# Optimization experiments

Measured on AMD Instinct MI355X. Metric: run time of the kernel, lower is better.

The kernel has to match this reference:

```python
import jax, jax.numpy as jnp
import numpy as np

IN_F, OUT_F = 4096, 4096
RANK, N_EXP, TOP_K = 8, 64, 16
R_DIM = 16
ALPHA = 32
SCALING = ALPHA / TOP_K  # 2.0
B_SZ, SEQ = 4, 4096
BOTTLENECK = N_EXP * RANK  # 512


def setup_inputs() -> dict:
    key = jax.random.key(0)
    kx, ka, kb, kq, kk = jax.random.split(key, 5)
    x = jax.random.normal(kx, (B_SZ, SEQ, IN_F), dtype=jnp.float32)
    # A: kaiming-uniform-like; B: torch inits to zeros but we use small random
    # values so the output / gradients are non-degenerate for kernel testing.
    A_w = jax.random.normal(ka, (BOTTLENECK, IN_F), dtype=jnp.float32) * (1.0 / np.sqrt(IN_F))
    B_w = jax.random.normal(kb, (OUT_F, BOTTLENECK), dtype=jnp.float32) * 0.02
    Wq_w = jax.random.normal(kq, (R_DIM, IN_F), dtype=jnp.float32) * (1.0 / np.sqrt(IN_F))
    keys = jax.random.normal(kk, (N_EXP, R_DIM), dtype=jnp.float32) * 0.01
    return {"x": x, "A_w": A_w, "B_w": B_w, "Wq_w": Wq_w, "keys": keys}


def reference(x, A_w, B_w, Wq_w, keys):
    # dropout p=0 -> identity
    # shared A projection: [b,s,d] @ [d, E*r] -> [b,s,E,r]
    z = jnp.einsum('bsd,ed->bse', x, A_w).reshape(B_SZ, SEQ, N_EXP, RANK)
    # lowrank router: scores = (x @ Wq.T) @ keys.T -> [b,s,E]
    q = jnp.einsum('bsd,rd->bsr', x, Wq_w)
    scores = jnp.einsum('bsr,er->bse', q, keys)
    top_scores, top_idx = jax.lax.top_k(scores, TOP_K)          # [b,s,k]
    top_w = jax.nn.softmax(top_scores, axis=-1)                  # [b,s,k]
    # dense gate [b,s,E] via scatter of softmaxed top-k weights
    gate = jnp.sum(jax.nn.one_hot(top_idx, N_EXP, dtype=top_w.dtype)
                   * top_w[..., None], axis=-2)                  # [b,s,E]
    z_gated = (z * gate[..., None]).reshape(B_SZ, SEQ, BOTTLENECK)
    out = jnp.einsum('bse,oe->bso', z_gated, B_w) * SCALING      # [b,s,out]
    return out
```

## Files before the change

kernel.cpp:

```cpp
#include <hip/hip_runtime.h>
#include <hip/hip_bf16.h>
#include <stdint.h>

#define T_TOK   16384
#define INF     4096
#define OUTF    4096
#define NEXP    64
#define TOPK    16
#define RDIM    16
#define BOT     512

typedef float  f32x4  __attribute__((ext_vector_type(4)));
typedef short  bf16x8 __attribute__((ext_vector_type(8)));

__device__ __forceinline__ unsigned short f2bf(float f) {
    union { float f; unsigned int u; } c; c.f = f;
    unsigned int r = c.u + 0x7fffu + ((c.u >> 16) & 1u);
    return (unsigned short)(r >> 16);
}

__device__ __forceinline__ void gld_lds16(const void* g, void* l) {
    __builtin_amdgcn_global_load_lds(
        (const __attribute__((address_space(1))) unsigned int*)(uintptr_t)g,
        (__attribute__((address_space(3))) unsigned int*)(unsigned int)(uintptr_t)l,
        16, 0, 0);
}

__global__ void __launch_bounds__(256) cast_w(const float* __restrict__ A,
                                              const float* __restrict__ B,
                                              unsigned short* __restrict__ Ab,
                                              unsigned short* __restrict__ Bb) {
    int i = blockIdx.x * 256 + threadIdx.x;
    const int nA = (BOT * INF) / 4;
    const float* src; unsigned short* dst; int k;
    if (i < nA) { src = A; dst = Ab; k = i; }
    else        { src = B; dst = Bb; k = i - nA; }
    f32x4 v = ((const f32x4*)src)[k];
    ushort4 o;
    o.x = f2bf(v.x); o.y = f2bf(v.y); o.z = f2bf(v.z); o.w = f2bf(v.w);
    ((ushort4*)dst)[k] = o;
}

#define RTM 4

__global__ void __launch_bounds__(256) router_kernel(
    const float* __restrict__ x,
    const float* __restrict__ Wq,
    const float* __restrict__ keys,
    unsigned short* __restrict__ xb,
    float* __restrict__ gate)
{
    const int tid  = threadIdx.x;
    const int lane = tid & 63;
    const int wave = tid >> 6;
    const int g    = blockIdx.x * 4 + wave;
    const size_t t0 = (size_t)g * RTM;

    float acc[RDIM][RTM] = {};

    const float*   xp = x  + t0 * INF + lane * 4;
    const float*   wp = Wq + lane * 4;
    unsigned short* xo = xb + t0 * INF + lane * 4;

    #pragma unroll 2
    for (int j = 0; j < 16; ++j) {
        const int d = j * 256;
        f32x4 xv[RTM];
        #pragma unroll
        for (int t = 0; t < RTM; ++t)
            xv[t] = *(const f32x4*)(xp + (size_t)t * INF + d);
        #pragma unroll
        for (int t = 0; t < RTM; ++t) {
            ushort4 bv;
            bv.x = f2bf(xv[t].x); bv.y = f2bf(xv[t].y);
            bv.z = f2bf(xv[t].z); bv.w = f2bf(xv[t].w);
            *(ushort4*)(xo + (size_t)t * INF + d) = bv;
        }
        #pragma unroll
        for (int rh = 0; rh < 2; ++rh) {
            f32x4 wv[8];
            #pragma unroll
            for (int r = 0; r < 8; ++r)
                wv[r] = *(const f32x4*)(wp + (size_t)(rh * 8 + r) * INF + d);
            #pragma unroll
            for (int r = 0; r < 8; ++r) {
                #pragma unroll
                for (int t = 0; t < RTM; ++t)
                    acc[rh * 8 + r][t] += wv[r].x * xv[t].x + wv[r].y * xv[t].y
                                        + wv[r].z * xv[t].z + wv[r].w * xv[t].w;
            }
        }
    }

    #pragma unroll
    for (int off = 1; off < 64; off <<= 1) {
        #pragma unroll
        for (int r = 0; r < RDIM; ++r)
            #pragma unroll
            for (int t = 0; t < RTM; ++t)
                acc[r][t] += __shfl_xor(acc[r][t], off, 64);
    }

    f32x4 kreg[4];
    #pragma unroll
    for (int i = 0; i < 4; ++i)
        kreg[i] = *(const f32x4*)&keys[lane * RDIM + i * 4];

    #pragma unroll
    for (int t = 0; t < RTM; ++t) {
        float s = 0.0f;
        #pragma unroll
        for (int i = 0; i < 4; ++i) {
            s += acc[i*4+0][t] * kreg[i].x + acc[i*4+1][t] * kreg[i].y
               + acc[i*4+2][t] * kreg[i].z + acc[i*4+3][t] * kreg[i].w;
        }
        int rank = 0;
        for (int j = 0; j < 64; ++j) {
            float sj = __shfl(s, j, 64);
            rank += (sj > s || (sj == s && j < lane)) ? 1 : 0;
        }
        float m = s;
        #pragma unroll
        for (int off = 32; off > 0; off >>= 1)
            m = fmaxf(m, __shfl_xor(m, off, 64));
        float e = (rank < TOPK) ? __expf(s - m) : 0.0f;
        float sum = e;
        #pragma unroll
        for (int off = 32; off > 0; off >>= 1)
            sum += __shfl_xor(sum, off, 64);
        gate[(t0 + t) * NEXP + lane] = e / sum;
    }
}

__global__ void __launch_bounds__(256) gemm_sk(
    const unsigned short* __restrict__ A,
    const unsigned short* __restrict__ Bm,
    float* __restrict__ Cp,
    const int M, const int N, const int K)
{
    constexpr int BM = 128, BN = 128, BK = 32, KSPLIT = 2;
    __shared__ __align__(16) unsigned short As[BM * BK];
    __shared__ __align__(16) unsigned short Bs[BN * BK];

    const int flat = blockIdx.x;
    const int wg   = (flat & 7) * 128 + (flat >> 3);
    const int bx   = wg & 3;
    const int ks   = (wg >> 2) & (KSPLIT - 1);
    const int by   = wg >> 3;

    const int tid  = threadIdx.x;
    const int lane = tid & 63;
    const int wave = tid >> 6;
    const int wr = wave >> 1, wc = wave & 1;
    const int bm = by * BM;
    const int bn = bx * BN;
    const int kchunk = K / KSPLIT;

    f32x4 acc[4][4] = {};

    const int srow = tid >> 2;
    const int scol = (tid & 3) * 8;
    const unsigned short* Ap = A  + (size_t)(bm + srow) * K + ks * kchunk + scol;
    const unsigned short* Bp = Bm + (size_t)(bn + srow) * K + ks * kchunk + scol;
    unsigned short* AsP = &As[tid * 8];
    unsigned short* BsP = &Bs[tid * 8];

    const int fm = lane & 15;
    const int fk = (lane >> 4) * 8;

    for (int k0 = 0; k0 < kchunk; k0 += BK) {
        __syncthreads();
        gld_lds16(Ap,                  AsP);
        gld_lds16(Ap + (size_t)64 * K, AsP + 64 * BK);
        gld_lds16(Bp,                  BsP);
        gld_lds16(Bp + (size_t)64 * K, BsP + 64 * BK);
        Ap += BK; Bp += BK;
        __syncthreads();

        bf16x8 af[4], bfr[4];
        #pragma unroll
        for (int i = 0; i < 4; ++i)
            af[i] = *(const bf16x8*)&As[(wr * 64 + i * 16 + fm) * BK + fk];
        #pragma unroll
        for (int j = 0; j < 4; ++j)
            bfr[j] = *(const bf16x8*)&Bs[(wc * 64 + j * 16 + fm) * BK + fk];
        #pragma unroll
        for (int i = 0; i < 4; ++i)
            #pragma unroll
            for (int j = 0; j < 4; ++j)
                acc[i][j] = __builtin_amdgcn_mfma_f32_16x16x32_bf16(af[i], bfr[j], acc[i][j], 0, 0, 0);
    }

    const int row0 = (lane >> 4) * 4;
    const int col  = lane & 15;
    float* Cpo = Cp + (size_t)ks * M * N;
    #pragma unroll
    for (int i = 0; i < 4; ++i) {
        #pragma unroll
        for (int j = 0; j < 4; ++j) {
            const int nn = bn + wc * 64 + j * 16 + col;
            #pragma unroll
            for (int r = 0; r < 4; ++r) {
                const int mm = bm + wr * 64 + i * 16 + row0 + r;
                Cpo[(size_t)mm * N + nn] = acc[i][j][r];
            }
        }
    }
}

__global__ void __launch_bounds__(256) reduce_gate_k(
    const float* __restrict__ Cp,
    const float* __restrict__ gate,
    unsigned short* __restrict__ Zg)
{
    const size_t i = (size_t)blockIdx.x * 256 + threadIdx.x;
    f32x4 v = ((const f32x4*)Cp)[i];
    f32x4 w = ((const f32x4*)(Cp + (size_t)T_TOK * BOT))[i];
    const int m = (int)(i >> 7);
    const int e = ((int)i & 127) >> 1;
    const float g = gate[(size_t)m * NEXP + e];
    ushort4 o;
    o.x = f2bf((v.x + w.x) * g);
    o.y = f2bf((v.y + w.y) * g);
    o.z = f2bf((v.z + w.z) * g);
    o.w = f2bf((v.w + w.w) * g);
    ((ushort4*)Zg)[i] = o;
}

template <int EPI>
__global__ void __launch_bounds__(256) gemm_bt(
    const unsigned short* __restrict__ A,
    const unsigned short* __restrict__ Bm,
    const float* __restrict__ gate,
    unsigned short* __restrict__ Cb,
    float* __restrict__ Cf,
    const int M, const int N, const int K)
{
    constexpr int BM = 128, BN = 128, BK = 32;
    __shared__ __align__(16) unsigned short As[BM * BK];
    __shared__ __align__(16) unsigned short Bs[BN * BK];

    const int tid  = threadIdx.x;
    const int lane = tid & 63;
    const int wave = tid >> 6;
    const int wr = wave >> 1, wc = wave & 1;
    const int bm = blockIdx.y * BM;
    const int bn = blockIdx.x * BN;

    f32x4 acc[4][4] = {};

    const int srow = tid >> 2;
    const int scol = (tid & 3) * 8;
    const unsigned short* Ap = A  + (size_t)(bm + srow) * K + scol;
    const unsigned short* Bp = Bm + (size_t)(bn + srow) * K + scol;
    unsigned short* AsP = &As[tid * 8];
    unsigned short* BsP = &Bs[tid * 8];

    const int fm = lane & 15;
    const int fk = (lane >> 4) * 8;

    for (int k0 = 0; k0 < K; k0 += BK) {
        __syncthreads();
        gld_lds16(Ap,                  AsP);
        gld_lds16(Ap + (size_t)64 * K, AsP + 64 * BK);
        gld_lds16(Bp,                  BsP);
        gld_lds16(Bp + (size_t)64 * K, BsP + 64 * BK);
        Ap += BK; Bp += BK;
        __syncthreads();

        bf16x8 af[4], bfr[4];
        #pragma unroll
        for (int i = 0; i < 4; ++i)
            af[i] = *(const bf16x8*)&As[(wr * 64 + i * 16 + fm) * BK + fk];
        #pragma unroll
        for (int j = 0; j < 4; ++j)
            bfr[j] = *(const bf16x8*)&Bs[(wc * 64 + j * 16 + fm) * BK + fk];
        #pragma unroll
        for (int i = 0; i < 4; ++i)
            #pragma unroll
            for (int j = 0; j < 4; ++j)
                acc[i][j] = __builtin_amdgcn_mfma_f32_16x16x32_bf16(af[i], bfr[j], acc[i][j], 0, 0, 0);
    }

    const int row0 = (lane >> 4) * 4;
    const int col  = lane & 15;
    #pragma unroll
    for (int i = 0; i < 4; ++i) {
        #pragma unroll
        for (int j = 0; j < 4; ++j) {
            const int nn = bn + wc * 64 + j * 16 + col;
            #pragma unroll
            for (int r = 0; r < 4; ++r) {
                const int mm = bm + wr * 64 + i * 16 + row0 + r;
                if (EPI == 0) {
                    float g = gate[(size_t)mm * NEXP + (nn >> 3)];
                    Cb[(size_t)mm * N + nn] = f2bf(acc[i][j][r] * g);
                } else {
                    Cf[(size_t)mm * N + nn] = acc[i][j][r] * 2.0f;
                }
            }
        }
    }
}

extern "C" void kernel_launch(void* const* d_in, const int* in_sizes, int n_in,
                              void* d_out, int out_size, void* d_ws, size_t ws_size,
                              hipStream_t stream) {
    const float* x    = (const float*)d_in[0];
    const float* A_w  = (const float*)d_in[1];
    const float* B_w  = (const float*)d_in[2];
    const float* Wq   = (const float*)d_in[3];
    const float* keys = (const float*)d_in[4];
    float* out = (float*)d_out;

    char* ws = (char*)d_ws;
    unsigned short* xb = (unsigned short*)(ws);
    unsigned short* Ab = (unsigned short*)(ws + 134217728);
    unsigned short* Bb = (unsigned short*)(ws + 138412032);
    float*        gate = (float*)        (ws + 142606336);
    unsigned short* Zg = (unsigned short*)(ws + 146800640);

    float* Cp = out;

    cast_w<<<dim3(4096), dim3(256), 0, stream>>>(A_w, B_w, Ab, Bb);
    router_kernel<<<dim3(T_TOK / (RTM * 4)), dim3(256), 0, stream>>>(x, Wq, keys, xb, gate);
    gemm_sk<<<dim3(1024), dim3(256), 0, stream>>>(xb, Ab, Cp, T_TOK, BOT, INF);
    reduce_gate_k<<<dim3(T_TOK * BOT / 4 / 256), dim3(256), 0, stream>>>(Cp, gate, Zg);
    gemm_bt<1><<<dim3(OUTF / 128, T_TOK / 128), dim3(256), 0, stream>>>(
        Zg, Bb, nullptr, nullptr, out, T_TOK, OUTF, BOT);
}
```

Before: 722.6 us.

## Fuse x bf16 cast into split-K GEMM A-load and fold scaling into B

The router no longer writes a bf16 copy of x. Instead the first split-K GEMM reads fp32 x directly, converts it to bf16 in registers and stores it into LDS, which removes a 128MB write and its later re-read. The SCALING factor of 2 is folded into the bf16 cast of B_w, so the final GEMM epilogue drops its multiply, and the router's rank loop gets an unroll pragma. In exchange, the GEMM A-tile loads become synchronous register loads rather than direct global-to-LDS copies, and x is read twice at fp32 width (once by the router, once by the GEMM).

```diff
diff --git a/kernel.cpp b/kernel.cpp
--- a/kernel.cpp
+++ b/kernel.cpp
@@ -12,6 +12,7 @@
 
 typedef float  f32x4  __attribute__((ext_vector_type(4)));
 typedef short  bf16x8 __attribute__((ext_vector_type(8)));
+typedef unsigned short u16x8 __attribute__((ext_vector_type(8)));
 
 __device__ __forceinline__ unsigned short f2bf(float f) {
     union { float f; unsigned int u; } c; c.f = f;
@@ -32,12 +33,13 @@
                                               unsigned short* __restrict__ Bb) {
     int i = blockIdx.x * 256 + threadIdx.x;
     const int nA = (BOT * INF) / 4;
-    const float* src; unsigned short* dst; int k;
-    if (i < nA) { src = A; dst = Ab; k = i; }
-    else        { src = B; dst = Bb; k = i - nA; }
+    float sc; const float* src; unsigned short* dst; int k;
+    if (i < nA) { src = A; dst = Ab; k = i;      sc = 1.0f; }
+    else        { src = B; dst = Bb; k = i - nA; sc = 2.0f; }
     f32x4 v = ((const f32x4*)src)[k];
     ushort4 o;
-    o.x = f2bf(v.x); o.y = f2bf(v.y); o.z = f2bf(v.z); o.w = f2bf(v.w);
+    o.x = f2bf(v.x * sc); o.y = f2bf(v.y * sc);
+    o.z = f2bf(v.z * sc); o.w = f2bf(v.w * sc);
     ((ushort4*)dst)[k] = o;
 }
 
@@ -47,7 +49,6 @@
     const float* __restrict__ x,
     const float* __restrict__ Wq,
     const float* __restrict__ keys,
-    unsigned short* __restrict__ xb,
     float* __restrict__ gate)
 {
     const int tid  = threadIdx.x;
@@ -58,9 +59,8 @@
 
     float acc[RDIM][RTM] = {};
 
-    const float*   xp = x  + t0 * INF + lane * 4;
-    const float*   wp = Wq + lane * 4;
-    unsigned short* xo = xb + t0 * INF + lane * 4;
+    const float* xp = x  + t0 * INF + lane * 4;
+    const float* wp = Wq + lane * 4;
 
     #pragma unroll 2
     for (int j = 0; j < 16; ++j) {
@@ -69,13 +69,6 @@
         #pragma unroll
         for (int t = 0; t < RTM; ++t)
             xv[t] = *(const f32x4*)(xp + (size_t)t * INF + d);
-        #pragma unroll
-        for (int t = 0; t < RTM; ++t) {
-            ushort4 bv;
-            bv.x = f2bf(xv[t].x); bv.y = f2bf(xv[t].y);
-            bv.z = f2bf(xv[t].z); bv.w = f2bf(xv[t].w);
-            *(ushort4*)(xo + (size_t)t * INF + d) = bv;
-        }
         #pragma unroll
         for (int rh = 0; rh < 2; ++rh) {
             f32x4 wv[8];
@@ -115,6 +108,7 @@
                + acc[i*4+2][t] * kreg[i].z + acc[i*4+3][t] * kreg[i].w;
         }
         int rank = 0;
+        #pragma unroll
         for (int j = 0; j < 64; ++j) {
             float sj = __shfl(s, j, 64);
             rank += (sj > s || (sj == s && j < lane)) ? 1 : 0;
@@ -133,7 +127,7 @@
 }
 
 __global__ void __launch_bounds__(256) gemm_sk(
-    const unsigned short* __restrict__ A,
+    const float* __restrict__ X,
     const unsigned short* __restrict__ Bm,
     float* __restrict__ Cp,
     const int M, const int N, const int K)
@@ -160,8 +154,8 @@
 
     const int srow = tid >> 2;
     const int scol = (tid & 3) * 8;
-    const unsigned short* Ap = A  + (size_t)(bm + srow) * K + ks * kchunk + scol;
-    const unsigned short* Bp = Bm + (size_t)(bn + srow) * K + ks * kchunk + scol;
+    const float*          Axp = X  + (size_t)(bm + srow) * K + ks * kchunk + scol;
+    const unsigned short* Bp  = Bm + (size_t)(bn + srow) * K + ks * kchunk + scol;
     unsigned short* AsP = &As[tid * 8];
     unsigned short* BsP = &Bs[tid * 8];
 
@@ -170,11 +164,20 @@
 
     for (int k0 = 0; k0 < kchunk; k0 += BK) {
         __syncthreads();
-        gld_lds16(Ap,                  AsP);
-        gld_lds16(Ap + (size_t)64 * K, AsP + 64 * BK);
         gld_lds16(Bp,                  BsP);
         gld_lds16(Bp + (size_t)64 * K, BsP + 64 * BK);
-        Ap += BK; Bp += BK;
+        f32x4 a0 = *(const f32x4*)(Axp);
+        f32x4 a1 = *(const f32x4*)(Axp + 4);
+        f32x4 a2 = *(const f32x4*)(Axp + (size_t)64 * K);
+        f32x4 a3 = *(const f32x4*)(Axp + (size_t)64 * K + 4);
+        u16x8 pa, pb;
+        pa[0]=f2bf(a0.x); pa[1]=f2bf(a0.y); pa[2]=f2bf(a0.z); pa[3]=f2bf(a0.w);
+        pa[4]=f2bf(a1.x); pa[5]=f2bf(a1.y); pa[6]=f2bf(a1.z); pa[7]=f2bf(a1.w);
+        pb[0]=f2bf(a2.x); pb[1]=f2bf(a2.y); pb[2]=f2bf(a2.z); pb[3]=f2bf(a2.w);
+        pb[4]=f2bf(a3.x); pb[5]=f2bf(a3.y); pb[6]=f2bf(a3.z); pb[7]=f2bf(a3.w);
+        *(u16x8*)(AsP)           = pa;
+        *(u16x8*)(AsP + 64 * BK) = pb;
+        Axp += BK; Bp += BK;
         __syncthreads();
 
         bf16x8 af[4], bfr[4];
@@ -227,12 +230,9 @@
     ((ushort4*)Zg)[i] = o;
 }
 
-template <int EPI>
 __global__ void __launch_bounds__(256) gemm_bt(
     const unsigned short* __restrict__ A,
     const unsigned short* __restrict__ Bm,
-    const float* __restrict__ gate,
-    unsigned short* __restrict__ Cb,
     float* __restrict__ Cf,
     const int M, const int N, const int K)
 {
@@ -292,12 +292,7 @@
             #pragma unroll
             for (int r = 0; r < 4; ++r) {
                 const int mm = bm + wr * 64 + i * 16 + row0 + r;
-                if (EPI == 0) {
-                    float g = gate[(size_t)mm * NEXP + (nn >> 3)];
-                    Cb[(size_t)mm * N + nn] = f2bf(acc[i][j][r] * g);
-                } else {
-                    Cf[(size_t)mm * N + nn] = acc[i][j][r] * 2.0f;
-                }
+                Cf[(size_t)mm * N + nn] = acc[i][j][r];
             }
         }
     }
@@ -314,18 +309,17 @@
     float* out = (float*)d_out;
 
     char* ws = (char*)d_ws;
-    unsigned short* xb = (unsigned short*)(ws);
-    unsigned short* Ab = (unsigned short*)(ws + 134217728);
-    unsigned short* Bb = (unsigned short*)(ws + 138412032);
-    float*        gate = (float*)        (ws + 142606336);
-    unsigned short* Zg = (unsigned short*)(ws + 146800640);
+    unsigned short* Ab = (unsigned short*)(ws);
+    unsigned short* Bb = (unsigned short*)(ws + 4194304);
+    float*        gate = (float*)        (ws + 8388608);
+    unsigned short* Zg = (unsigned short*)(ws + 12582912);
 
     float* Cp = out;
 
     cast_w<<<dim3(4096), dim3(256), 0, stream>>>(A_w, B_w, Ab, Bb);
-    router_kernel<<<dim3(T_TOK / (RTM * 4)), dim3(256), 0, stream>>>(x, Wq, keys, xb, gate);
-    gemm_sk<<<dim3(1024), dim3(256), 0, stream>>>(xb, Ab, Cp, T_TOK, BOT, INF);
+    router_kernel<<<dim3(T_TOK / (RTM * 4)), dim3(256), 0, stream>>>(x, Wq, keys, gate);
+    gemm_sk<<<dim3(1024), dim3(256), 0, stream>>>(x, Ab, Cp, T_TOK, BOT, INF);
     reduce_gate_k<<<dim3(T_TOK * BOT / 4 / 256), dim3(256), 0, stream>>>(Cp, gate, Zg);
-    gemm_bt<1><<<dim3(OUTF / 128, T_TOK / 128), dim3(256), 0, stream>>>(
-        Zg, Bb, nullptr, nullptr, out, T_TOK, OUTF, BOT);
-}
+    gemm_bt<<<dim3(OUTF / 128, T_TOK / 128), dim3(256), 0, stream>>>(
+        Zg, Bb, out, T_TOK, OUTF, BOT);
+}
```

New measurement: 756.1 us. +4.6%, slower.
